# Kernel tuning notes

Measured on AMD Instinct MI355X. Metric: run time of the kernel, lower is better.

Reference implementation:

```python
import jax, jax.numpy as jnp
import numpy as np

B_SZ, L, D, N = 2, 2048, 1024, 16


def setup_inputs() -> dict:
    key = jax.random.key(0)
    ks = jax.random.split(key, 8)
    x = jax.random.normal(ks[0], (B_SZ, L, D), dtype=jnp.float32)
    # torch.nn.Linear params: weight [out, in], bias [out]; y = x @ W.T + b
    s1 = 1.0 / np.sqrt(D)
    W1 = jax.random.uniform(ks[1], (D, D), minval=-s1, maxval=s1, dtype=jnp.float32)
    b1 = jax.random.uniform(ks[2], (D,), minval=-s1, maxval=s1, dtype=jnp.float32)
    W2 = jax.random.uniform(ks[3], (N, D), minval=-s1, maxval=s1, dtype=jnp.float32)
    b2 = jax.random.uniform(ks[4], (N,), minval=-s1, maxval=s1, dtype=jnp.float32)
    W3 = jax.random.uniform(ks[5], (N, D), minval=-s1, maxval=s1, dtype=jnp.float32)
    b3 = jax.random.uniform(ks[6], (N,), minval=-s1, maxval=s1, dtype=jnp.float32)
    # A: xavier_uniform on (D, N)
    lim = np.sqrt(6.0 / (D + N))
    A = jax.random.uniform(ks[7], (D, N), minval=-lim, maxval=lim, dtype=jnp.float32)
    return {"x": x, "W1": W1, "b1": b1, "W2": W2, "b2": b2, "W3": W3, "b3": b3, "A": A}


def reference(x, W1, b1, W2, b2, W3, b3, A):
    # delta = softplus(fc1(x)); B = fc2(x); C = fc3(x)
    delta = jax.nn.softplus(x @ W1.T + b1)          # [b, l, d]
    Bm = x @ W2.T + b2                               # [b, l, n]
    Cm = x @ W3.T + b3                               # [b, l, n]
    # discretization: dB = einsum('bld,bln->bldn', delta, B)
    dB = jnp.einsum('bld,bln->bldn', delta, Bm)      # [b, l, d, n]
    # dA = exp(einsum('bld,dn->bldn', delta, A)) is computed in the source but
    # multiplies a zero-initialized h, so it does not affect the output.
    # h = dA*0 + x[..., None] * dB
    h = x[..., None] * dB                            # [b, l, d, n]
    y = jnp.einsum('bln,bldn->bld', Cm, h)           # [b, l, d]
    return y
```

## Files before the change

### kernel.cpp

```cpp
#include <hip/hip_runtime.h>
#include <hip/hip_bf16.h>
#include <math.h>


typedef __bf16 bf16x8 __attribute__((ext_vector_type(8)));
typedef __bf16 bf16x4 __attribute__((ext_vector_type(4)));
typedef float  f32x4  __attribute__((ext_vector_type(4)));

#define MDIM 4096
#define KDIM 1024
#define NDIM 1024

__device__ __forceinline__ void async16(const void* g, void* l) {
    __builtin_amdgcn_global_load_lds(
        (const __attribute__((address_space(1))) void*)g,
        (__attribute__((address_space(3))) void*)l, 16, 0, 0);
}

__device__ __forceinline__ float softplus_f(float z) {
    return fmaxf(z, 0.f) + log1pf(__expf(-fabsf(z)));
}

__device__ __forceinline__ bf16x8 cvt8(float4 v0, float4 v1) {
    bf16x8 h = { (__bf16)v0.x, (__bf16)v0.y, (__bf16)v0.z, (__bf16)v0.w,
                 (__bf16)v1.x, (__bf16)v1.y, (__bf16)v1.z, (__bf16)v1.w };
    return h;
}

__global__ __launch_bounds__(256)
void prep2(const float* __restrict__ x, const float* __restrict__ W1,
           const float* __restrict__ W2, const float* __restrict__ b2,
           const float* __restrict__ W3, const float* __restrict__ b3,
           __bf16* __restrict__ xb, __bf16* __restrict__ w1b,
           float* __restrict__ s) {
    __shared__ __align__(16) __bf16 xs[16 * 1032];
    __shared__ float red[4][2][16][16];
    const int t = threadIdx.x;
    const int wave = t >> 6, lane = t & 63;
    const int lrow = lane & 15, quad = lane >> 4;
    const size_t m0 = (size_t)blockIdx.x * 16;
    const int wk0 = wave * 256;

    {
        const float4* src = reinterpret_cast<const float4*>(W1) + (size_t)blockIdx.x * 1024;
        bf16x4* dst = reinterpret_cast<bf16x4*>(w1b) + (size_t)blockIdx.x * 1024;
#pragma unroll
        for (int i = 0; i < 4; ++i) {
            float4 v = src[i * 256 + t];
            bf16x4 h = { (__bf16)v.x, (__bf16)v.y, (__bf16)v.z, (__bf16)v.w };
            dst[i * 256 + t] = h;
        }
    }

#pragma unroll
    for (int i = 0; i < 16; ++i) {
        float4 v = *reinterpret_cast<const float4*>(x + (m0 + i) * KDIM + t * 4);
        bf16x4 h = { (__bf16)v.x, (__bf16)v.y, (__bf16)v.z, (__bf16)v.w };
        *reinterpret_cast<bf16x4*>(&xs[i * 1032 + t * 4]) = h;
        *reinterpret_cast<bf16x4*>(xb + (m0 + i) * KDIM + t * 4) = h;
    }
    __syncthreads();

    f32x4 acc[2] = {};
#pragma unroll
    for (int ks = 0; ks < 256; ks += 32) {
        bf16x8 a = *reinterpret_cast<const bf16x8*>(
            &xs[lrow * 1032 + wk0 + ks + quad * 8]);
        {
            const float* p2 = W2 + (size_t)lrow * KDIM + wk0 + ks + quad * 8;
            float4 v0 = *reinterpret_cast<const float4*>(p2);
            float4 v1 = *reinterpret_cast<const float4*>(p2 + 4);
            acc[0] = __builtin_amdgcn_mfma_f32_16x16x32_bf16(a, cvt8(v0, v1), acc[0], 0, 0, 0);
        }
        {
            const float* p3 = W3 + (size_t)lrow * KDIM + wk0 + ks + quad * 8;
            float4 v0 = *reinterpret_cast<const float4*>(p3);
            float4 v1 = *reinterpret_cast<const float4*>(p3 + 4);
            acc[1] = __builtin_amdgcn_mfma_f32_16x16x32_bf16(a, cvt8(v0, v1), acc[1], 0, 0, 0);
        }
    }
#pragma unroll
    for (int r = 0; r < 4; ++r) {
        red[wave][0][quad * 4 + r][lrow] = acc[0][r];
        red[wave][1][quad * 4 + r][lrow] = acc[1][r];
    }
    __syncthreads();

    {
        const int row = t >> 4, n = t & 15;
        float Bv = red[0][0][row][n] + red[1][0][row][n]
                 + red[2][0][row][n] + red[3][0][row][n] + b2[n];
        float Cv = red[0][1][row][n] + red[1][1][row][n]
                 + red[2][1][row][n] + red[3][1][row][n] + b3[n];
        float p = Bv * Cv;
        p += __shfl_xor(p, 1);
        p += __shfl_xor(p, 2);
        p += __shfl_xor(p, 4);
        p += __shfl_xor(p, 8);
        if (n == 0) s[m0 + row] = p;
    }
}

#define GBM 128
#define GBN 64
#define GBK 128
__global__ __launch_bounds__(512, 4)
void gemm_bf(const __bf16* __restrict__ xb, const __bf16* __restrict__ w1b,
             const float* __restrict__ x, const float* __restrict__ b1,
             const float* __restrict__ s, float* __restrict__ y) {
    __shared__ __align__(16) __bf16 As[GBM * GBK];
    __shared__ __align__(16) __bf16 Bs[GBN * GBK];
    const int nwg = gridDim.x * gridDim.y;
    const int cpx = nwg >> 3;
    const int bid0 = blockIdx.y * gridDim.x + blockIdx.x;
    const int bid = (bid0 & 7) * cpx + (bid0 >> 3);
    const int bm = bid >> 4, bn = bid & 15;
    const int t = threadIdx.x;
    const int wave = t >> 6, lane = t & 63;
    const int wm = (wave >> 1) * 32, wn = (wave & 1) * 32;
    const int lrow = lane & 15, quad = lane >> 4;
    const int sr  = lane >> 4;
    const int pcg = lane & 15;
    const size_t m0 = (size_t)bm * GBM, n0 = (size_t)bn * GBN;

    f32x4 acc[2][2] = {};

    for (int k0 = 0; k0 < KDIM; k0 += GBK) {
#pragma unroll
        for (int i = 0; i < 4; ++i) {
            int q = wave * 4 + i;
            int row = q * 4 + sr;
            int lcg = pcg ^ (row & 15);
            async16(xb + (m0 + row) * KDIM + k0 + lcg * 8, &As[q * 512]);
        }
#pragma unroll
        for (int i = 0; i < 2; ++i) {
            int q = wave * 2 + i;
            int row = q * 4 + sr;
            int lcg = pcg ^ (row & 15);
            async16(w1b + (n0 + row) * KDIM + k0 + lcg * 8, &Bs[q * 512]);
        }
        __syncthreads();

#pragma unroll
        for (int kk = 0; kk < GBK; kk += 32) {
            const int cg = (kk >> 3) + quad;
            bf16x8 af[2], bfr[2];
#pragma unroll
            for (int mi = 0; mi < 2; ++mi) {
                int row = wm + mi * 16 + lrow;
                af[mi] = *reinterpret_cast<const bf16x8*>(
                    &As[row * GBK + ((cg ^ (row & 15)) << 3)]);
            }
#pragma unroll
            for (int ni = 0; ni < 2; ++ni) {
                int row = wn + ni * 16 + lrow;
                bfr[ni] = *reinterpret_cast<const bf16x8*>(
                    &Bs[row * GBK + ((cg ^ (row & 15)) << 3)]);
            }
#pragma unroll
            for (int mi = 0; mi < 2; ++mi)
#pragma unroll
                for (int ni = 0; ni < 2; ++ni)
                    acc[mi][ni] = __builtin_amdgcn_mfma_f32_16x16x32_bf16(
                        af[mi], bfr[ni], acc[mi][ni], 0, 0, 0);
        }
        __syncthreads();
    }

#pragma unroll
    for (int ni = 0; ni < 2; ++ni) {
        const size_t gn = n0 + wn + ni * 16 + lrow;
        const float bias = b1[gn];
#pragma unroll
        for (int mi = 0; mi < 2; ++mi) {
#pragma unroll
            for (int r = 0; r < 4; ++r) {
                const size_t gm = m0 + wm + mi * 16 + quad * 4 + r;
                float z = acc[mi][ni][r] + bias;
                y[gm * NDIM + gn] = x[gm * NDIM + gn] * softplus_f(z) * s[gm];
            }
        }
    }
}

__global__ __launch_bounds__(256)
void s_kernel_fb(const float* __restrict__ x,
                 const float* __restrict__ W2, const float* __restrict__ b2,
                 const float* __restrict__ W3, const float* __restrict__ b3,
                 float* __restrict__ s) {
    __shared__ float xs[1024];
    __shared__ float ps[8][32];
    __shared__ float bc[32];
    const int m = blockIdx.x;
    const int t = threadIdx.x;
    reinterpret_cast<float4*>(xs)[t] =
        reinterpret_cast<const float4*>(x + (size_t)m * 1024)[t];
    __syncthreads();
    const int n = t & 15;
    const int mat = (t >> 4) & 1;
    const int seg = t >> 5;
    const float* __restrict__ W = mat ? W3 : W2;
    const float* __restrict__ wr = W + (size_t)n * 1024 + seg * 128;
    const float* __restrict__ xr = xs + seg * 128;
    float p = 0.f;
#pragma unroll
    for (int i = 0; i < 128; i += 4) {
        float4 w4 = *reinterpret_cast<const float4*>(wr + i);
        float4 x4 = *reinterpret_cast<const float4*>(xr + i);
        p += w4.x * x4.x + w4.y * x4.y + w4.z * x4.z + w4.w * x4.w;
    }
    ps[seg][t & 31] = p;
    __syncthreads();
    if (t < 32) {
        float tot = 0.f;
#pragma unroll
        for (int g = 0; g < 8; ++g) tot += ps[g][t];
        tot += (t < 16) ? b2[t] : b3[t - 16];
        bc[t] = tot;
    }
    __syncthreads();
    if (t == 0) {
        float ss = 0.f;
#pragma unroll
        for (int nn = 0; nn < 16; ++nn) ss += bc[nn] * bc[16 + nn];
        s[m] = ss;
    }
}

#define BM 128
#define BN 64
#define BK 64
#define LDK 72
__global__ __launch_bounds__(256)
void gemm_fused_fb(const float* __restrict__ x, const float* __restrict__ W1,
                   const float* __restrict__ b1, const float* __restrict__ s,
                   float* __restrict__ y) {
    __shared__ __align__(16) __bf16 As[BM * LDK];
    __shared__ __align__(16) __bf16 Bs[BN * LDK];
    const int bm = blockIdx.y;
    const int bn = blockIdx.x;
    const int t = threadIdx.x;
    const int wave = t >> 6;
    const int lane = t & 63;
    const int wm = (wave >> 1) * 64;
    const int wn = (wave & 1) * 32;
    const int lrow = lane & 15;
    const int quad = lane >> 4;
    f32x4 acc[4][2] = {};
    const int rbase = t >> 4;
    const int scol = (t & 15) * 4;
    const float* __restrict__ xg = x + (size_t)(bm * BM) * KDIM + scol;
    const float* __restrict__ wg = W1 + (size_t)(bn * BN) * KDIM + scol;
    for (int k0 = 0; k0 < KDIM; k0 += BK) {
#pragma unroll
        for (int rr = 0; rr < 8; ++rr) {
            int row = rr * 16 + rbase;
            float4 v = *reinterpret_cast<const float4*>(xg + (size_t)row * KDIM + k0);
            bf16x4 h = { (__bf16)v.x, (__bf16)v.y, (__bf16)v.z, (__bf16)v.w };
            *reinterpret_cast<bf16x4*>(&As[row * LDK + scol]) = h;
        }
#pragma unroll
        for (int rr = 0; rr < 4; ++rr) {
            int row = rr * 16 + rbase;
            float4 v = *reinterpret_cast<const float4*>(wg + (size_t)row * KDIM + k0);
            bf16x4 h = { (__bf16)v.x, (__bf16)v.y, (__bf16)v.z, (__bf16)v.w };
            *reinterpret_cast<bf16x4*>(&Bs[row * LDK + scol]) = h;
        }
        __syncthreads();
#pragma unroll
        for (int kk = 0; kk < BK; kk += 32) {
            bf16x8 af[4];
            bf16x8 bfr[2];
#pragma unroll
            for (int mi = 0; mi < 4; ++mi)
                af[mi] = *reinterpret_cast<const bf16x8*>(
                    &As[(wm + mi * 16 + lrow) * LDK + kk + quad * 8]);
#pragma unroll
            for (int ni = 0; ni < 2; ++ni)
                bfr[ni] = *reinterpret_cast<const bf16x8*>(
                    &Bs[(wn + ni * 16 + lrow) * LDK + kk + quad * 8]);
#pragma unroll
            for (int mi = 0; mi < 4; ++mi)
#pragma unroll
                for (int ni = 0; ni < 2; ++ni)
                    acc[mi][ni] = __builtin_amdgcn_mfma_f32_16x16x32_bf16(
                        af[mi], bfr[ni], acc[mi][ni], 0, 0, 0);
        }
        __syncthreads();
    }
    const int gmb = bm * BM + wm;
    const int gnb = bn * BN + wn;
#pragma unroll
    for (int ni = 0; ni < 2; ++ni) {
        const int gn = gnb + ni * 16 + lrow;
        const float bias = b1[gn];
#pragma unroll
        for (int mi = 0; mi < 4; ++mi) {
            const int gm0 = gmb + mi * 16 + quad * 4;
#pragma unroll
            for (int r = 0; r < 4; ++r) {
                const int gm = gm0 + r;
                float z = acc[mi][ni][r] + bias;
                y[(size_t)gm * NDIM + gn] =
                    x[(size_t)gm * NDIM + gn] * softplus_f(z) * s[gm];
            }
        }
    }
}

extern "C" void kernel_launch(void* const* d_in, const int* in_sizes, int n_in,
                              void* d_out, int out_size, void* d_ws, size_t ws_size,
                              hipStream_t stream) {
    const float* x  = (const float*)d_in[0];
    const float* W1 = (const float*)d_in[1];
    const float* b1 = (const float*)d_in[2];
    const float* W2 = (const float*)d_in[3];
    const float* b2 = (const float*)d_in[4];
    const float* W3 = (const float*)d_in[5];
    const float* b3 = (const float*)d_in[6];

    float* y = (float*)d_out;

    const size_t XB_BYTES = (size_t)MDIM * KDIM * 2;
    const size_t WB_BYTES = (size_t)NDIM * KDIM * 2;
    const size_t S_BYTES  = (size_t)MDIM * 4;

    if (ws_size >= XB_BYTES + WB_BYTES + S_BYTES) {
        __bf16* xb  = (__bf16*)d_ws;
        __bf16* w1b = (__bf16*)((char*)d_ws + XB_BYTES);
        float*  s   = (float*)((char*)d_ws + XB_BYTES + WB_BYTES);
        prep2<<<dim3(MDIM / 16), dim3(256), 0, stream>>>(
            x, W1, W2, b2, W3, b3, xb, w1b, s);
        gemm_bf<<<dim3(NDIM / GBN, MDIM / GBM), dim3(512), 0, stream>>>(
            xb, w1b, x, b1, s, y);
    } else {
        float* s = (float*)d_ws;
        s_kernel_fb<<<dim3(MDIM), dim3(256), 0, stream>>>(x, W2, b2, W3, b3, s);
        gemm_fused_fb<<<dim3(NDIM / BN, MDIM / BM), dim3(256), 0, stream>>>(x, W1, b1, s, y);
    }
}
```

Baseline: 111.0 us.

## Double-buffer GEMM K tiles and halve rows per prep block

The bf16 GEMM now uses two 64-wide K stages in shared memory. It issues the async global-to-LDS load for the next stage before computing on the current one, so load latency can overlap the MFMA work, with an XOR swizzle adapted to 8 chunks. The prep kernel handles 8 rows per block instead of 16, which doubles the grid so the conversion and the B·C reduction are spread across more workgroups. The cost is more barriers per K and half-utilised MFMA rows in prep.

```diff
diff --git a/kernel.cpp b/kernel.cpp
--- a/kernel.cpp
+++ b/kernel.cpp
@@ -33,19 +33,19 @@
            const float* __restrict__ W3, const float* __restrict__ b3,
            __bf16* __restrict__ xb, __bf16* __restrict__ w1b,
            float* __restrict__ s) {
-    __shared__ __align__(16) __bf16 xs[16 * 1032];
+    __shared__ __align__(16) __bf16 xs[8 * 1032];
     __shared__ float red[4][2][16][16];
     const int t = threadIdx.x;
     const int wave = t >> 6, lane = t & 63;
     const int lrow = lane & 15, quad = lane >> 4;
-    const size_t m0 = (size_t)blockIdx.x * 16;
+    const size_t m0 = (size_t)blockIdx.x * 8;
     const int wk0 = wave * 256;
 
     {
-        const float4* src = reinterpret_cast<const float4*>(W1) + (size_t)blockIdx.x * 1024;
-        bf16x4* dst = reinterpret_cast<bf16x4*>(w1b) + (size_t)blockIdx.x * 1024;
-#pragma unroll
-        for (int i = 0; i < 4; ++i) {
+        const float4* src = reinterpret_cast<const float4*>(W1) + (size_t)blockIdx.x * 512;
+        bf16x4* dst = reinterpret_cast<bf16x4*>(w1b) + (size_t)blockIdx.x * 512;
+#pragma unroll
+        for (int i = 0; i < 2; ++i) {
             float4 v = src[i * 256 + t];
             bf16x4 h = { (__bf16)v.x, (__bf16)v.y, (__bf16)v.z, (__bf16)v.w };
             dst[i * 256 + t] = h;
@@ -53,7 +53,7 @@
     }
 
 #pragma unroll
-    for (int i = 0; i < 16; ++i) {
+    for (int i = 0; i < 8; ++i) {
         float4 v = *reinterpret_cast<const float4*>(x + (m0 + i) * KDIM + t * 4);
         bf16x4 h = { (__bf16)v.x, (__bf16)v.y, (__bf16)v.z, (__bf16)v.w };
         *reinterpret_cast<bf16x4*>(&xs[i * 1032 + t * 4]) = h;
@@ -65,7 +65,7 @@
 #pragma unroll
     for (int ks = 0; ks < 256; ks += 32) {
         bf16x8 a = *reinterpret_cast<const bf16x8*>(
-            &xs[lrow * 1032 + wk0 + ks + quad * 8]);
+            &xs[(lrow & 7) * 1032 + wk0 + ks + quad * 8]);
         {
             const float* p2 = W2 + (size_t)lrow * KDIM + wk0 + ks + quad * 8;
             float4 v0 = *reinterpret_cast<const float4*>(p2);
@@ -86,7 +86,7 @@
     }
     __syncthreads();
 
-    {
+    if (t < 128) {
         const int row = t >> 4, n = t & 15;
         float Bv = red[0][0][row][n] + red[1][0][row][n]
                  + red[2][0][row][n] + red[3][0][row][n] + b2[n];
@@ -103,13 +103,15 @@
 
 #define GBM 128
 #define GBN 64
-#define GBK 128
+#define GBK 64
+#define A_ELEMS (GBM * GBK)
+#define B_ELEMS (GBN * GBK)
 __global__ __launch_bounds__(512, 4)
 void gemm_bf(const __bf16* __restrict__ xb, const __bf16* __restrict__ w1b,
              const float* __restrict__ x, const float* __restrict__ b1,
              const float* __restrict__ s, float* __restrict__ y) {
-    __shared__ __align__(16) __bf16 As[GBM * GBK];
-    __shared__ __align__(16) __bf16 Bs[GBN * GBK];
+    __shared__ __align__(16) __bf16 As[2 * A_ELEMS];
+    __shared__ __align__(16) __bf16 Bs[2 * B_ELEMS];
     const int nwg = gridDim.x * gridDim.y;
     const int cpx = nwg >> 3;
     const int bid0 = blockIdx.y * gridDim.x + blockIdx.x;
@@ -119,29 +121,33 @@
     const int wave = t >> 6, lane = t & 63;
     const int wm = (wave >> 1) * 32, wn = (wave & 1) * 32;
     const int lrow = lane & 15, quad = lane >> 4;
-    const int sr  = lane >> 4;
-    const int pcg = lane & 15;
+    const int shi = lane >> 3;
+    const int spc = lane & 7;
     const size_t m0 = (size_t)bm * GBM, n0 = (size_t)bn * GBN;
 
     f32x4 acc[2][2] = {};
 
-    for (int k0 = 0; k0 < KDIM; k0 += GBK) {
-#pragma unroll
-        for (int i = 0; i < 4; ++i) {
-            int q = wave * 4 + i;
-            int row = q * 4 + sr;
-            int lcg = pcg ^ (row & 15);
-            async16(xb + (m0 + row) * KDIM + k0 + lcg * 8, &As[q * 512]);
-        }
+    auto stage = [&](int buf, int k0) {
+        __bf16* Ad = As + buf * A_ELEMS;
+        __bf16* Bd = Bs + buf * B_ELEMS;
 #pragma unroll
         for (int i = 0; i < 2; ++i) {
-            int q = wave * 2 + i;
-            int row = q * 4 + sr;
-            int lcg = pcg ^ (row & 15);
-            async16(w1b + (n0 + row) * KDIM + k0 + lcg * 8, &Bs[q * 512]);
-        }
-        __syncthreads();
-
+            int j = wave * 2 + i;
+            int row = j * 8 + shi;
+            int lcg = spc ^ (row & 7);
+            async16(xb + (m0 + row) * KDIM + k0 + lcg * 8, Ad + j * 512);
+        }
+        {
+            int j = wave;
+            int row = j * 8 + shi;
+            int lcg = spc ^ (row & 7);
+            async16(w1b + (n0 + row) * KDIM + k0 + lcg * 8, Bd + j * 512);
+        }
+    };
+
+    auto compute = [&](int buf) {
+        const __bf16* Ac = As + buf * A_ELEMS;
+        const __bf16* Bc = Bs + buf * B_ELEMS;
 #pragma unroll
         for (int kk = 0; kk < GBK; kk += 32) {
             const int cg = (kk >> 3) + quad;
@@ -150,13 +156,13 @@
             for (int mi = 0; mi < 2; ++mi) {
                 int row = wm + mi * 16 + lrow;
                 af[mi] = *reinterpret_cast<const bf16x8*>(
-                    &As[row * GBK + ((cg ^ (row & 15)) << 3)]);
+                    &Ac[row * GBK + ((cg ^ (row & 7)) << 3)]);
             }
 #pragma unroll
             for (int ni = 0; ni < 2; ++ni) {
                 int row = wn + ni * 16 + lrow;
                 bfr[ni] = *reinterpret_cast<const bf16x8*>(
-                    &Bs[row * GBK + ((cg ^ (row & 15)) << 3)]);
+                    &Bc[row * GBK + ((cg ^ (row & 7)) << 3)]);
             }
 #pragma unroll
             for (int mi = 0; mi < 2; ++mi)
@@ -165,6 +171,17 @@
                     acc[mi][ni] = __builtin_amdgcn_mfma_f32_16x16x32_bf16(
                         af[mi], bfr[ni], acc[mi][ni], 0, 0, 0);
         }
+    };
+
+    stage(0, 0);
+    __syncthreads();
+#pragma unroll 1
+    for (int k0 = 0; k0 < KDIM; k0 += 2 * GBK) {
+        if (k0 + GBK < KDIM) stage(1, k0 + GBK);
+        compute(0);
+        __syncthreads();
+        if (k0 + 2 * GBK < KDIM) stage(0, k0 + 2 * GBK);
+        compute(1);
         __syncthreads();
     }
 
@@ -330,7 +347,7 @@
         __bf16* xb  = (__bf16*)d_ws;
         __bf16* w1b = (__bf16*)((char*)d_ws + XB_BYTES);
         float*  s   = (float*)((char*)d_ws + XB_BYTES + WB_BYTES);
-        prep2<<<dim3(MDIM / 16), dim3(256), 0, stream>>>(
+        prep2<<<dim3(MDIM / 8), dim3(256), 0, stream>>>(
             x, W1, W2, b2, W3, b3, xb, w1b, s);
         gemm_bf<<<dim3(NDIM / GBN, MDIM / GBM), dim3(512), 0, stream>>>(
             xb, w1b, x, b1, s, y);
```

Measured after the change: 118.6 us. +6.8%, slower.
